# Performance work log

Hardware: AMD Instinct MI355X
Metric: run time of the kernel (lower is better)

The kernel has to match this reference:

```python
import jax, jax.numpy as jnp
import numpy as np

N_EMBD = 384
N_HEAD = 6
HEAD_SIZE = N_EMBD // N_HEAD  # 64
BLOCK = 64
EPS = 1e-5


def _layernorm(x, g, b):
    mu = jnp.mean(x, axis=-1, keepdims=True)
    var = jnp.mean(jnp.square(x - mu), axis=-1, keepdims=True)
    return (x - mu) * jax.lax.rsqrt(var + EPS) * g + b


def setup_inputs() -> dict:
    key = jax.random.key(0)
    ks = jax.random.split(key, 12)
    s = 0.02
    return {
        "x": jax.random.normal(ks[0], (1024, BLOCK, N_EMBD), dtype=jnp.float32),
        "ln1_g": jnp.ones((N_EMBD,), jnp.float32),
        "ln1_b": jnp.zeros((N_EMBD,), jnp.float32),
        "Wq": jax.random.normal(ks[1], (N_HEAD, N_EMBD, HEAD_SIZE), jnp.float32) * s,
        "Wk": jax.random.normal(ks[2], (N_HEAD, N_EMBD, HEAD_SIZE), jnp.float32) * s,
        "Wv": jax.random.normal(ks[3], (N_HEAD, N_EMBD, HEAD_SIZE), jnp.float32) * s,
        "Wo": jax.random.normal(ks[4], (N_EMBD, N_EMBD), jnp.float32) * s,
        "bo": jnp.zeros((N_EMBD,), jnp.float32),
        "ln2_g": jnp.ones((N_EMBD,), jnp.float32),
        "ln2_b": jnp.zeros((N_EMBD,), jnp.float32),
        "W1": jax.random.normal(ks[5], (N_EMBD, 4 * N_EMBD), jnp.float32) * s,
        "b1": jnp.zeros((4 * N_EMBD,), jnp.float32),
        "W2": jax.random.normal(ks[6], (4 * N_EMBD, N_EMBD), jnp.float32) * s,
        "b2": jnp.zeros((N_EMBD,), jnp.float32),
    }


def reference(x, ln1_g, ln1_b, Wq, Wk, Wv, Wo, bo, ln2_g, ln2_b, W1, b1, W2, b2):
    B, T, C = x.shape
    # --- multi-head causal self-attention on ln1(x) ---
    xn = _layernorm(x, ln1_g, ln1_b)
    q = jnp.einsum('btc,hcd->bhtd', xn, Wq)
    k = jnp.einsum('btc,hcd->bhtd', xn, Wk)
    v = jnp.einsum('btc,hcd->bhtd', xn, Wv)
    scale = HEAD_SIZE ** -0.5
    att = jnp.einsum('bhtd,bhsd->bhts', q, k) * scale
    causal = jnp.tril(jnp.ones((T, T), bool))
    att = jnp.where(causal, att, -jnp.inf)
    att = jax.nn.softmax(att, axis=-1)  # dropout is identity at eval
    out = jnp.einsum('bhts,bhsd->bhtd', att, v)
    out = out.transpose(0, 2, 1, 3).reshape(B, T, C)  # concat heads
    x = x + out @ Wo + bo
    # --- feed-forward on ln2(x) ---
    xn2 = _layernorm(x, ln2_g, ln2_b)
    h = jax.nn.relu(xn2 @ W1 + b1)
    x = x + h @ W2 + b2
    return x
```

## Files before the change

### kernel.cpp

```cpp
#include <hip/hip_runtime.h>

#define TT 64
#define CC 384
#define NH 6
#define HID 1536
#define LDX 392
#define LDH 72
#define LDM 200

typedef __bf16 bf16x8 __attribute__((ext_vector_type(8)));
typedef float f32x4 __attribute__((ext_vector_type(4)));
typedef unsigned short us8 __attribute__((ext_vector_type(8)));

#define MFMA(a, b, c) __builtin_amdgcn_mfma_f32_16x16x32_bf16(a, b, c, 0, 0, 0)

static __device__ __forceinline__ unsigned short f2bf(float f) {
  unsigned u = __builtin_bit_cast(unsigned, f);
  u += 0x7FFFu + ((u >> 16) & 1u);
  return (unsigned short)(u >> 16);
}
static __device__ __forceinline__ float bf2f(unsigned short h) {
  unsigned u = ((unsigned)h) << 16;
  return __builtin_bit_cast(float, u);
}
static __device__ __forceinline__ bf16x8 ld8(const unsigned short* p) {
  return __builtin_bit_cast(bf16x8, *reinterpret_cast<const us8*>(p));
}

__global__ void prep_w(const float* __restrict__ Wq, const float* __restrict__ Wk,
                       const float* __restrict__ Wv, const float* __restrict__ Wo,
                       const float* __restrict__ W1, const float* __restrict__ W2,
                       unsigned short* __restrict__ ws) {
  const int T0 = 1152 * 384;
  const int T1 = T0 + 384 * 384;
  const int T2 = T1 + 1536 * 384;
  const int T3 = T2 + 384 * 1536;
  for (int i = blockIdx.x * blockDim.x + threadIdx.x; i < T3; i += gridDim.x * blockDim.x) {
    float v;
    if (i < T0) {
      int n = i / 384, k = i % 384;
      int hh = n / 192, j = n % 192;
      const float* W = (j < 64) ? Wq : (j < 128) ? Wk : Wv;
      int d = (j < 64) ? j : (j < 128) ? j - 64 : j - 128;
      v = W[((size_t)hh * 384 + k) * 64 + d];
    } else if (i < T1) {
      int i2 = i - T0; int n = i2 / 384, k = i2 % 384;
      v = Wo[(size_t)k * 384 + n];
    } else if (i < T2) {
      int i2 = i - T1; int n = i2 / 384, k = i2 % 384;
      v = W1[(size_t)k * 1536 + n];
    } else {
      int i2 = i - T2; int n = i2 / 1536, k = i2 % 1536;
      v = W2[(size_t)k * 384 + n];
    }
    ws[i] = f2bf(v);
  }
}

__global__ __launch_bounds__(256, 2)
void attn_fwd(const float* __restrict__ x,
              const float* __restrict__ ln1g, const float* __restrict__ ln1b,
              const float* __restrict__ bo,
              const unsigned short* __restrict__ Wqkv,
              const unsigned short* __restrict__ WoT,
              float* __restrict__ x2) {
  __shared__ unsigned short sXN[TT * LDX];
  __shared__ unsigned short sHEAD[3 * TT * LDH];
  unsigned short* sQ = sHEAD;
  unsigned short* sK = sHEAD + TT * LDH;
  unsigned short* sV = sHEAD + 2 * TT * LDH;

  const int b = blockIdx.x;
  const int tid = threadIdx.x;
  const int wv = tid >> 6;
  const int ln = tid & 63;
  const int l16 = ln & 15;
  const int lg = ln >> 4;
  const float* xb = x + (size_t)b * TT * CC;
  const f32x4 Z4 = {0.f, 0.f, 0.f, 0.f};

#pragma unroll 1
  for (int r = wv * 16; r < wv * 16 + 16; ++r) {
    float v[6], s = 0.f, sq = 0.f;
#pragma unroll
    for (int j = 0; j < 6; ++j) { v[j] = xb[r * CC + ln + 64 * j]; s += v[j]; sq += v[j] * v[j]; }
#pragma unroll
    for (int off = 32; off; off >>= 1) { s += __shfl_xor(s, off); sq += __shfl_xor(sq, off); }
    float mu = s * (1.f / CC);
    float rs = rsqrtf(sq * (1.f / CC) - mu * mu + 1e-5f);
#pragma unroll
    for (int j = 0; j < 6; ++j) {
      int c = ln + 64 * j;
      sXN[r * LDX + c] = f2bf((v[j] - mu) * rs * ln1g[c] + ln1b[c]);
    }
  }
  __syncthreads();

  f32x4 pacc[4][6];
#pragma unroll
  for (int m = 0; m < 4; ++m)
#pragma unroll
    for (int c = 0; c < 6; ++c) pacc[m][c] = Z4;

  const unsigned short* prow[6];
#pragma unroll
  for (int c = 0; c < 6; ++c)
    prow[c] = WoT + (size_t)(wv * 96 + c * 16 + l16) * CC + 8 * lg;

#pragma unroll 1
  for (int h = 0; h < NH; ++h) {
    const unsigned short* wrow[3];
#pragma unroll
    for (int c = 0; c < 3; ++c)
      wrow[c] = Wqkv + (size_t)(h * 192 + wv * 48 + c * 16 + l16) * CC + 8 * lg;

    f32x4 qacc[4][3];
#pragma unroll
    for (int m = 0; m < 4; ++m)
#pragma unroll
      for (int c = 0; c < 3; ++c) qacc[m][c] = Z4;

    bf16x8 bpre[2][3];
#pragma unroll
    for (int c = 0; c < 3; ++c) bpre[0][c] = ld8(wrow[c] + 0);
#pragma unroll
    for (int c = 0; c < 3; ++c) bpre[1][c] = ld8(wrow[c] + 32);
#pragma unroll
    for (int kk = 0; kk < CC; kk += 32) {
      const int slot = (kk >> 5) & 1;
      bf16x8 bcur[3];
#pragma unroll
      for (int c = 0; c < 3; ++c) bcur[c] = bpre[slot][c];
      if (kk + 64 < CC) {
#pragma unroll
        for (int c = 0; c < 3; ++c) bpre[slot][c] = ld8(wrow[c] + kk + 64);
      }
      bf16x8 a[4];
#pragma unroll
      for (int m = 0; m < 4; ++m)
        a[m] = ld8(&sXN[(m * 16 + l16) * LDX + kk + 8 * lg]);
      __builtin_amdgcn_s_setprio(1);
#pragma unroll
      for (int c = 0; c < 3; ++c)
#pragma unroll
        for (int m = 0; m < 4; ++m) qacc[m][c] = MFMA(a[m], bcur[c], qacc[m][c]);
      __builtin_amdgcn_s_setprio(0);
    }
    __syncthreads();
#pragma unroll
    for (int m = 0; m < 4; ++m)
#pragma unroll
      for (int c = 0; c < 3; ++c) {
        int n = wv * 48 + c * 16 + l16;
#pragma unroll
        for (int rg = 0; rg < 4; ++rg) {
          int t = m * 16 + lg * 4 + rg;
          unsigned short bv = f2bf(qacc[m][c][rg]);
          if (n < 64) sQ[t * LDH + n] = bv;
          else if (n < 128) sK[t * LDH + (n - 64)] = bv;
          else sV[(n - 128) * LDH + t] = bv;
        }
      }
    __syncthreads();

    f32x4 sacc[4];
#pragma unroll
    for (int c = 0; c < 4; ++c) sacc[c] = Z4;
#pragma unroll
    for (int kk = 0; kk < 64; kk += 32) {
      bf16x8 a = ld8(&sQ[(wv * 16 + l16) * LDH + kk + 8 * lg]);
#pragma unroll
      for (int c = 0; c < 4; ++c) {
        bf16x8 bb = ld8(&sK[(c * 16 + l16) * LDH + kk + 8 * lg]);
        sacc[c] = MFMA(a, bb, sacc[c]);
      }
    }
#pragma unroll
    for (int rg = 0; rg < 4; ++rg) {
      int row = wv * 16 + lg * 4 + rg;
      float e[4], mx = -1e30f;
#pragma unroll
      for (int c = 0; c < 4; ++c) {
        int col = c * 16 + l16;
        float vv = sacc[c][rg] * 0.125f;
        e[c] = (col <= row) ? vv : -1e30f;
        mx = fmaxf(mx, e[c]);
      }
#pragma unroll
      for (int off = 8; off; off >>= 1) mx = fmaxf(mx, __shfl_xor(mx, off));
      float sum = 0.f;
#pragma unroll
      for (int c = 0; c < 4; ++c) {
        int col = c * 16 + l16;
        e[c] = (col <= row) ? __expf(e[c] - mx) : 0.f;
        sum += e[c];
      }
#pragma unroll
      for (int off = 8; off; off >>= 1) sum += __shfl_xor(sum, off);
      float inv = 1.f / sum;
#pragma unroll
      for (int c = 0; c < 4; ++c)
        sQ[row * LDH + c * 16 + l16] = f2bf(e[c] * inv);
    }

    bf16x8 pb[2][6];
#pragma unroll
    for (int s2 = 0; s2 < 2; ++s2)
#pragma unroll
      for (int c = 0; c < 6; ++c)
        pb[s2][c] = ld8(prow[c] + h * 64 + 32 * s2);

    f32x4 oacc[4];
#pragma unroll
    for (int c = 0; c < 4; ++c) oacc[c] = Z4;
#pragma unroll
    for (int kk = 0; kk < 64; kk += 32) {
      bf16x8 a = ld8(&sQ[(wv * 16 + l16) * LDH + kk + 8 * lg]);
#pragma unroll
      for (int c = 0; c < 4; ++c) {
        bf16x8 bb = ld8(&sV[(c * 16 + l16) * LDH + kk + 8 * lg]);
        oacc[c] = MFMA(a, bb, oacc[c]);
      }
    }
    __syncthreads();
#pragma unroll
    for (int c = 0; c < 4; ++c)
#pragma unroll
      for (int rg = 0; rg < 4; ++rg) {
        int t = wv * 16 + lg * 4 + rg;
        sK[t * LDH + c * 16 + l16] = f2bf(oacc[c][rg]);
      }
    __syncthreads();

    __builtin_amdgcn_s_setprio(1);
#pragma unroll
    for (int kk = 0; kk < 64; kk += 32) {
      const int slot = kk >> 5;
      bf16x8 a[4];
#pragma unroll
      for (int m = 0; m < 4; ++m)
        a[m] = ld8(&sK[(m * 16 + l16) * LDH + kk + 8 * lg]);
#pragma unroll
      for (int c = 0; c < 6; ++c)
#pragma unroll
        for (int m = 0; m < 4; ++m) pacc[m][c] = MFMA(a[m], pb[slot][c], pacc[m][c]);
    }
    __builtin_amdgcn_s_setprio(0);
  }

  float* xo = x2 + (size_t)b * TT * CC;
#pragma unroll
  for (int m = 0; m < 4; ++m)
#pragma unroll
    for (int c = 0; c < 6; ++c) {
      int n = wv * 96 + c * 16 + l16;
      float bov = bo[n];
#pragma unroll
      for (int rg = 0; rg < 4; ++rg) {
        int t = m * 16 + lg * 4 + rg;
        xo[t * CC + n] = xb[t * CC + n] + pacc[m][c][rg] + bov;
      }
    }
}

__global__ __launch_bounds__(256, 2)
void mlp_fwd(const float* __restrict__ ln2g, const float* __restrict__ ln2b,
             const float* __restrict__ b1, const float* __restrict__ b2,
             const unsigned short* __restrict__ W1T,
             const unsigned short* __restrict__ W2T,
             float* xo) {
  __shared__ unsigned short sXN[TT * LDX];
  __shared__ unsigned short sH[TT * LDM];

  const int b = blockIdx.x;
  const int tid = threadIdx.x;
  const int wv = tid >> 6;
  const int ln = tid & 63;
  const int l16 = ln & 15;
  const int lg = ln >> 4;
  float* xb = xo + (size_t)b * TT * CC;
  const f32x4 Z4 = {0.f, 0.f, 0.f, 0.f};

#pragma unroll 1
  for (int r = wv * 16; r < wv * 16 + 16; ++r) {
    float v[6], s = 0.f, sq = 0.f;
#pragma unroll
    for (int j = 0; j < 6; ++j) { v[j] = xb[r * CC + ln + 64 * j]; s += v[j]; sq += v[j] * v[j]; }
#pragma unroll
    for (int off = 32; off; off >>= 1) { s += __shfl_xor(s, off); sq += __shfl_xor(sq, off); }
    float mu = s * (1.f / CC);
    float rs = rsqrtf(sq * (1.f / CC) - mu * mu + 1e-5f);
#pragma unroll
    for (int j = 0; j < 6; ++j) {
      int c = ln + 64 * j;
      sXN[r * LDX + c] = f2bf((v[j] - mu) * rs * ln2g[c] + ln2b[c]);
    }
  }
  __syncthreads();

  f32x4 macc[4][6];
#pragma unroll
  for (int m = 0; m < 4; ++m)
#pragma unroll
    for (int c = 0; c < 6; ++c) macc[m][c] = Z4;

  const unsigned short* w2row[6];
#pragma unroll
  for (int c = 0; c < 6; ++c)
    w2row[c] = W2T + (size_t)(wv * 96 + c * 16 + l16) * HID + 8 * lg;

#pragma unroll 1
  for (int ch = 0; ch < 8; ++ch) {
    const unsigned short* w1row[3];
#pragma unroll
    for (int c = 0; c < 3; ++c)
      w1row[c] = W1T + (size_t)(ch * 192 + wv * 48 + c * 16 + l16) * CC + 8 * lg;

    f32x4 hacc[4][3];
#pragma unroll
    for (int m = 0; m < 4; ++m)
#pragma unroll
      for (int c = 0; c < 3; ++c) hacc[m][c] = Z4;

    bf16x8 bpre[2][3];
#pragma unroll
    for (int c = 0; c < 3; ++c) bpre[0][c] = ld8(w1row[c] + 0);
#pragma unroll
    for (int c = 0; c < 3; ++c) bpre[1][c] = ld8(w1row[c] + 32);
#pragma unroll
    for (int kk = 0; kk < CC; kk += 32) {
      const int slot = (kk >> 5) & 1;
      bf16x8 bcur[3];
#pragma unroll
      for (int c = 0; c < 3; ++c) bcur[c] = bpre[slot][c];
      if (kk + 64 < CC) {
#pragma unroll
        for (int c = 0; c < 3; ++c) bpre[slot][c] = ld8(w1row[c] + kk + 64);
      }
      bf16x8 a[4];
#pragma unroll
      for (int m = 0; m < 4; ++m)
        a[m] = ld8(&sXN[(m * 16 + l16) * LDX + kk + 8 * lg]);
      __builtin_amdgcn_s_setprio(1);
#pragma unroll
      for (int c = 0; c < 3; ++c)
#pragma unroll
        for (int m = 0; m < 4; ++m) hacc[m][c] = MFMA(a[m], bcur[c], hacc[m][c]);
      __builtin_amdgcn_s_setprio(0);
    }
    __syncthreads();
#pragma unroll
    for (int m = 0; m < 4; ++m)
#pragma unroll
      for (int c = 0; c < 3; ++c) {
        int nl = wv * 48 + c * 16 + l16;
        float b1v = b1[ch * 192 + nl];
#pragma unroll
        for (int rg = 0; rg < 4; ++rg) {
          int t = m * 16 + lg * 4 + rg;
          sH[t * LDM + nl] = f2bf(fmaxf(hacc[m][c][rg] + b1v, 0.f));
        }
      }
    __syncthreads();

    bf16x8 b2p[6];
#pragma unroll
    for (int c = 0; c < 6; ++c) b2p[c] = ld8(w2row[c] + ch * 192);
#pragma unroll
    for (int kk = 0; kk < 192; kk += 32) {
      bf16x8 b2n[6];
      if (kk + 32 < 192) {
#pragma unroll
        for (int c = 0; c < 6; ++c) b2n[c] = ld8(w2row[c] + ch * 192 + kk + 32);
      }
      bf16x8 a[4];
#pragma unroll
      for (int m = 0; m < 4; ++m)
        a[m] = ld8(&sH[(m * 16 + l16) * LDM + kk + 8 * lg]);
      __builtin_amdgcn_s_setprio(1);
#pragma unroll
      for (int c = 0; c < 6; ++c)
#pragma unroll
        for (int m = 0; m < 4; ++m) macc[m][c] = MFMA(a[m], b2p[c], macc[m][c]);
      __builtin_amdgcn_s_setprio(0);
      if (kk + 32 < 192) {
#pragma unroll
        for (int c = 0; c < 6; ++c) b2p[c] = b2n[c];
      }
    }
  }
#pragma unroll
  for (int m = 0; m < 4; ++m)
#pragma unroll
    for (int c = 0; c < 6; ++c) {
      int n = wv * 96 + c * 16 + l16;
      float b2v = b2[n];
#pragma unroll
      for (int rg = 0; rg < 4; ++rg) {
        int t = m * 16 + lg * 4 + rg;
        size_t idx = (size_t)t * CC + n;
        float x2v = xb[idx];
        xb[idx] = x2v + macc[m][c][rg] + b2v;
      }
    }
}

extern "C" void kernel_launch(void* const* d_in, const int* in_sizes, int n_in,
                              void* d_out, int out_size, void* d_ws, size_t ws_size,
                              hipStream_t stream) {
  const float* x    = (const float*)d_in[0];
  const float* ln1g = (const float*)d_in[1];
  const float* ln1b = (const float*)d_in[2];
  const float* Wq   = (const float*)d_in[3];
  const float* Wk   = (const float*)d_in[4];
  const float* Wv   = (const float*)d_in[5];
  const float* Wo   = (const float*)d_in[6];
  const float* bo   = (const float*)d_in[7];
  const float* ln2g = (const float*)d_in[8];
  const float* ln2b = (const float*)d_in[9];
  const float* W1   = (const float*)d_in[10];
  const float* b1   = (const float*)d_in[11];
  const float* W2   = (const float*)d_in[12];
  const float* b2   = (const float*)d_in[13];
  unsigned short* ws = (unsigned short*)d_ws;

  const size_t need = (size_t)(1152 * 384 + 384 * 384 + 1536 * 384 + 384 * 1536) * 2;
  if (ws_size < need) return;

  hipLaunchKernelGGL(prep_w, dim3(1024), dim3(256), 0, stream, Wq, Wk, Wv, Wo, W1, W2, ws);

  const unsigned short* Wqkv = ws;
  const unsigned short* WoT  = ws + 1152 * 384;
  const unsigned short* W1T  = WoT + 384 * 384;
  const unsigned short* W2T  = W1T + 1536 * 384;
  int nblk = in_sizes[0] / (TT * CC);

  hipLaunchKernelGGL(attn_fwd, dim3(nblk), dim3(256), 0, stream,
                     x, ln1g, ln1b, bo, Wqkv, WoT, (float*)d_out);
  hipLaunchKernelGGL(mlp_fwd, dim3(nblk), dim3(256), 0, stream,
                     ln2g, ln2b, b1, b2, W1T, W2T, (float*)d_out);
}
```

Baseline: 512.2 us.

## Restructure MLP kernel to 8 waves with double-buffered LDS weight staging

The MLP kernel moves from 4 to 8 waves per block and switches hidden chunks from 8×192 to 6×256. Weight tiles now stream through per-wave double-buffered LDS slots using global_load_lds with XOR-swizzled layout and explicit vmcnt waits, replacing direct register prefetch from global memory. The aim is to overlap weight fetches with MFMA work and raise latency hiding through more waves. In exchange the block uses much more LDS (an extra 64KB), which may limit occupancy. The s_setprio hints in the attention kernel are also removed.

```diff
diff --git a/kernel.cpp b/kernel.cpp
--- a/kernel.cpp
+++ b/kernel.cpp
@@ -6,13 +6,14 @@
 #define HID 1536
 #define LDX 392
 #define LDH 72
-#define LDM 200
+#define LDS_H 264
 
 typedef __bf16 bf16x8 __attribute__((ext_vector_type(8)));
 typedef float f32x4 __attribute__((ext_vector_type(4)));
 typedef unsigned short us8 __attribute__((ext_vector_type(8)));
 
 #define MFMA(a, b, c) __builtin_amdgcn_mfma_f32_16x16x32_bf16(a, b, c, 0, 0, 0)
+#define WAITVM(N) asm volatile("s_waitcnt vmcnt(" #N ")" ::: "memory")
 
 static __device__ __forceinline__ unsigned short f2bf(float f) {
   unsigned u = __builtin_bit_cast(unsigned, f);
@@ -25,6 +26,11 @@
 }
 static __device__ __forceinline__ bf16x8 ld8(const unsigned short* p) {
   return __builtin_bit_cast(bf16x8, *reinterpret_cast<const us8*>(p));
+}
+static __device__ __forceinline__ void glds16(const unsigned short* g, unsigned short* l) {
+  __builtin_amdgcn_global_load_lds(
+      (const __attribute__((address_space(1))) void*)g,
+      (__attribute__((address_space(3))) void*)l, 16, 0, 0);
 }
 
 __global__ void prep_w(const float* __restrict__ Wq, const float* __restrict__ Wk,
@@ -139,12 +145,10 @@
 #pragma unroll
       for (int m = 0; m < 4; ++m)
         a[m] = ld8(&sXN[(m * 16 + l16) * LDX + kk + 8 * lg]);
-      __builtin_amdgcn_s_setprio(1);
 #pragma unroll
       for (int c = 0; c < 3; ++c)
 #pragma unroll
         for (int m = 0; m < 4; ++m) qacc[m][c] = MFMA(a[m], bcur[c], qacc[m][c]);
-      __builtin_amdgcn_s_setprio(0);
     }
     __syncthreads();
 #pragma unroll
@@ -232,7 +236,6 @@
       }
     __syncthreads();
 
-    __builtin_amdgcn_s_setprio(1);
 #pragma unroll
     for (int kk = 0; kk < 64; kk += 32) {
       const int slot = kk >> 5;
@@ -245,7 +248,6 @@
 #pragma unroll
         for (int m = 0; m < 4; ++m) pacc[m][c] = MFMA(a[m], pb[slot][c], pacc[m][c]);
     }
-    __builtin_amdgcn_s_setprio(0);
   }
 
   float* xo = x2 + (size_t)b * TT * CC;
@@ -263,14 +265,15 @@
     }
 }
 
-__global__ __launch_bounds__(256, 2)
+__global__ __launch_bounds__(512, 2)
 void mlp_fwd(const float* __restrict__ ln2g, const float* __restrict__ ln2b,
              const float* __restrict__ b1, const float* __restrict__ b2,
              const unsigned short* __restrict__ W1T,
              const unsigned short* __restrict__ W2T,
              float* xo) {
   __shared__ unsigned short sXN[TT * LDX];
-  __shared__ unsigned short sH[TT * LDM];
+  __shared__ unsigned short sH[TT * LDS_H];
+  __shared__ unsigned short sW[8 * 4096];
 
   const int b = blockIdx.x;
   const int tid = threadIdx.x;
@@ -280,9 +283,10 @@
   const int lg = ln >> 4;
   float* xb = xo + (size_t)b * TT * CC;
   const f32x4 Z4 = {0.f, 0.f, 0.f, 0.f};
-
-#pragma unroll 1
-  for (int r = wv * 16; r < wv * 16 + 16; ++r) {
+  unsigned short* myW = sW + (wv << 12);
+
+#pragma unroll 1
+  for (int r = wv * 8; r < wv * 8 + 8; ++r) {
     float v[6], s = 0.f, sq = 0.f;
 #pragma unroll
     for (int j = 0; j < 6; ++j) { v[j] = xb[r * CC + ln + 64 * j]; s += v[j]; sq += v[j] * v[j]; }
@@ -298,102 +302,113 @@
   }
   __syncthreads();
 
-  f32x4 macc[4][6];
+  const int w1_row = (wv << 5) + (ln >> 3);
+  const int w1_kp0 = (((ln & 7) ^ (ln >> 3)) << 3);
+  const int w2_row = wv * 48 + (ln >> 2);
+  const int w2_kp0 = ((((ln & 3) ^ ((ln >> 3) & 3))) << 3);
+
+  f32x4 macc[4][3];
 #pragma unroll
   for (int m = 0; m < 4; ++m)
 #pragma unroll
-    for (int c = 0; c < 6; ++c) macc[m][c] = Z4;
-
-  const unsigned short* w2row[6];
-#pragma unroll
-  for (int c = 0; c < 6; ++c)
-    w2row[c] = W2T + (size_t)(wv * 96 + c * 16 + l16) * HID + 8 * lg;
-
-#pragma unroll 1
-  for (int ch = 0; ch < 8; ++ch) {
-    const unsigned short* w1row[3];
-#pragma unroll
-    for (int c = 0; c < 3; ++c)
-      w1row[c] = W1T + (size_t)(ch * 192 + wv * 48 + c * 16 + l16) * CC + 8 * lg;
-
-    f32x4 hacc[4][3];
+    for (int c = 0; c < 3; ++c) macc[m][c] = Z4;
+
+#pragma unroll 1
+  for (int ch = 0; ch < 6; ++ch) {
+    f32x4 hacc[4][2];
 #pragma unroll
     for (int m = 0; m < 4; ++m)
 #pragma unroll
-      for (int c = 0; c < 3; ++c) hacc[m][c] = Z4;
-
-    bf16x8 bpre[2][3];
-#pragma unroll
-    for (int c = 0; c < 3; ++c) bpre[0][c] = ld8(w1row[c] + 0);
-#pragma unroll
-    for (int c = 0; c < 3; ++c) bpre[1][c] = ld8(w1row[c] + 32);
-#pragma unroll
-    for (int kk = 0; kk < CC; kk += 32) {
-      const int slot = (kk >> 5) & 1;
-      bf16x8 bcur[3];
-#pragma unroll
-      for (int c = 0; c < 3; ++c) bcur[c] = bpre[slot][c];
-      if (kk + 64 < CC) {
-#pragma unroll
-        for (int c = 0; c < 3; ++c) bpre[slot][c] = ld8(w1row[c] + kk + 64);
-      }
-      bf16x8 a[4];
-#pragma unroll
-      for (int m = 0; m < 4; ++m)
-        a[m] = ld8(&sXN[(m * 16 + l16) * LDX + kk + 8 * lg]);
-      __builtin_amdgcn_s_setprio(1);
-#pragma unroll
-      for (int c = 0; c < 3; ++c)
-#pragma unroll
-        for (int m = 0; m < 4; ++m) hacc[m][c] = MFMA(a[m], bcur[c], hacc[m][c]);
-      __builtin_amdgcn_s_setprio(0);
-    }
-    __syncthreads();
+      for (int c = 0; c < 2; ++c) hacc[m][c] = Z4;
+
+    {
+      const unsigned short* g = W1T + (size_t)(ch * 256 + w1_row) * CC + 0 * 64 + w1_kp0;
+      unsigned short* d = myW + 0 * 2048;
+#pragma unroll
+      for (int j = 0; j < 4; ++j) glds16(g + (size_t)(j * 8) * CC, d + (j << 9));
+    }
+    int cb = 0;
+#pragma unroll 1
+    for (int s = 0; s < 6; ++s) {
+      if (s < 5) {
+        const unsigned short* g = W1T + (size_t)(ch * 256 + w1_row) * CC + (s + 1) * 64 + w1_kp0;
+        unsigned short* d = myW + (cb ^ 1) * 2048;
+#pragma unroll
+        for (int j = 0; j < 4; ++j) glds16(g + (size_t)(j * 8) * CC, d + (j << 9));
+        WAITVM(4);
+      } else {
+        WAITVM(0);
+      }
+#pragma unroll
+      for (int kk2 = 0; kk2 < 2; ++kk2) {
+        bf16x8 a[4];
+#pragma unroll
+        for (int m = 0; m < 4; ++m)
+          a[m] = ld8(&sXN[(m * 16 + l16) * LDX + s * 64 + kk2 * 32 + 8 * lg]);
+#pragma unroll
+        for (int c = 0; c < 2; ++c) {
+          int rloc = (c << 4) + l16;
+          bf16x8 bb = ld8(&myW[cb * 2048 + rloc * 64 + ((kk2 * 32 + 8 * lg) ^ ((l16 & 7) << 3))]);
+#pragma unroll
+          for (int m = 0; m < 4; ++m) hacc[m][c] = MFMA(a[m], bb, hacc[m][c]);
+        }
+      }
+      cb ^= 1;
+    }
+    __syncthreads();
+
+    {
+      const unsigned short* g = W2T + (size_t)w2_row * HID + ch * 256 + 0 * 32 + w2_kp0;
+      unsigned short* d = myW + 0 * 1536;
+#pragma unroll
+      for (int j = 0; j < 3; ++j) glds16(g + (size_t)(j * 16) * HID, d + (j << 9));
+    }
 #pragma unroll
     for (int m = 0; m < 4; ++m)
 #pragma unroll
-      for (int c = 0; c < 3; ++c) {
-        int nl = wv * 48 + c * 16 + l16;
-        float b1v = b1[ch * 192 + nl];
+      for (int c = 0; c < 2; ++c) {
+        int nl = (wv << 5) + (c << 4) + l16;
+        float b1v = b1[ch * 256 + nl];
 #pragma unroll
         for (int rg = 0; rg < 4; ++rg) {
           int t = m * 16 + lg * 4 + rg;
-          sH[t * LDM + nl] = f2bf(fmaxf(hacc[m][c][rg] + b1v, 0.f));
+          sH[t * LDS_H + nl] = f2bf(fmaxf(hacc[m][c][rg] + b1v, 0.f));
         }
       }
     __syncthreads();
 
-    bf16x8 b2p[6];
-#pragma unroll
-    for (int c = 0; c < 6; ++c) b2p[c] = ld8(w2row[c] + ch * 192);
-#pragma unroll
-    for (int kk = 0; kk < 192; kk += 32) {
-      bf16x8 b2n[6];
-      if (kk + 32 < 192) {
-#pragma unroll
-        for (int c = 0; c < 6; ++c) b2n[c] = ld8(w2row[c] + ch * 192 + kk + 32);
+    cb = 0;
+#pragma unroll 1
+    for (int s = 0; s < 8; ++s) {
+      if (s < 7) {
+        const unsigned short* g = W2T + (size_t)w2_row * HID + ch * 256 + (s + 1) * 32 + w2_kp0;
+        unsigned short* d = myW + (cb ^ 1) * 1536;
+#pragma unroll
+        for (int j = 0; j < 3; ++j) glds16(g + (size_t)(j * 16) * HID, d + (j << 9));
+        WAITVM(3);
+      } else {
+        WAITVM(0);
       }
       bf16x8 a[4];
 #pragma unroll
       for (int m = 0; m < 4; ++m)
-        a[m] = ld8(&sH[(m * 16 + l16) * LDM + kk + 8 * lg]);
-      __builtin_amdgcn_s_setprio(1);
-#pragma unroll
-      for (int c = 0; c < 6; ++c)
-#pragma unroll
-        for (int m = 0; m < 4; ++m) macc[m][c] = MFMA(a[m], b2p[c], macc[m][c]);
-      __builtin_amdgcn_s_setprio(0);
-      if (kk + 32 < 192) {
-#pragma unroll
-        for (int c = 0; c < 6; ++c) b2p[c] = b2n[c];
-      }
+        a[m] = ld8(&sH[(m * 16 + l16) * LDS_H + s * 32 + 8 * lg]);
+#pragma unroll
+      for (int c = 0; c < 3; ++c) {
+        int rloc = (c << 4) + l16;
+        bf16x8 bb = ld8(&myW[cb * 1536 + rloc * 32 + ((8 * lg) ^ (((rloc >> 1) & 3) << 3))]);
+#pragma unroll
+        for (int m = 0; m < 4; ++m) macc[m][c] = MFMA(a[m], bb, macc[m][c]);
+      }
+      cb ^= 1;
     }
   }
+
 #pragma unroll
   for (int m = 0; m < 4; ++m)
 #pragma unroll
-    for (int c = 0; c < 6; ++c) {
-      int n = wv * 96 + c * 16 + l16;
+    for (int c = 0; c < 3; ++c) {
+      int n = wv * 48 + c * 16 + l16;
       float b2v = b2[n];
 #pragma unroll
       for (int rg = 0; rg < 4; ++rg) {
@@ -437,6 +452,6 @@
 
   hipLaunchKernelGGL(attn_fwd, dim3(nblk), dim3(256), 0, stream,
                      x, ln1g, ln1b, bo, Wqkv, WoT, (float*)d_out);
-  hipLaunchKernelGGL(mlp_fwd, dim3(nblk), dim3(256), 0, stream,
+  hipLaunchKernelGGL(mlp_fwd, dim3(nblk), dim3(512), 0, stream,
                      ln2g, ln2b, b1, b2, W1T, W2T, (float*)d_out);
 }
```

Result: faster. 468.4 us (-8.6%).

## Restructure MLP kernel to 8 waves with swizzled LDS layout and smaller hidden chunks

Applied to the files above, without the earlier changes.

The MLP kernel moves from 4 to 8 waves per block (512 threads). Each wave now owns 16 hidden columns per 128-wide hidden chunk (12 chunks) and 48 output columns, which halves the per-wave accumulators and is meant to raise occupancy and latency hiding. The padded row-major LDS tiles become an XOR-swizzled fragment layout so the MFMA operand loads avoid bank conflicts. The trade-offs are more chunk iterations, more barriers per block, and each wave reloading the same A fragments from LDS.

```diff
diff --git a/kernel.cpp b/kernel.cpp
--- a/kernel.cpp
+++ b/kernel.cpp
@@ -6,7 +6,6 @@
 #define HID 1536
 #define LDX 392
 #define LDH 72
-#define LDM 200
 
 typedef __bf16 bf16x8 __attribute__((ext_vector_type(8)));
 typedef float f32x4 __attribute__((ext_vector_type(4)));
@@ -263,14 +262,14 @@
     }
 }
 
-__global__ __launch_bounds__(256, 2)
+__global__ __launch_bounds__(512, 4)
 void mlp_fwd(const float* __restrict__ ln2g, const float* __restrict__ ln2b,
              const float* __restrict__ b1, const float* __restrict__ b2,
              const unsigned short* __restrict__ W1T,
              const unsigned short* __restrict__ W2T,
              float* xo) {
-  __shared__ unsigned short sXN[TT * LDX];
-  __shared__ unsigned short sH[TT * LDM];
+  __shared__ unsigned short sXN[24576];
+  __shared__ unsigned short sH[8192];
 
   const int b = blockIdx.x;
   const int tid = threadIdx.x;
@@ -280,9 +279,10 @@
   const int lg = ln >> 4;
   float* xb = xo + (size_t)b * TT * CC;
   const f32x4 Z4 = {0.f, 0.f, 0.f, 0.f};
+  const int rx = (l16 ^ lg) << 3;
 
 #pragma unroll 1
-  for (int r = wv * 16; r < wv * 16 + 16; ++r) {
+  for (int r = wv * 8; r < wv * 8 + 8; ++r) {
     float v[6], s = 0.f, sq = 0.f;
 #pragma unroll
     for (int j = 0; j < 6; ++j) { v[j] = xb[r * CC + ln + 64 * j]; s += v[j]; sq += v[j] * v[j]; }
@@ -290,110 +290,99 @@
     for (int off = 32; off; off >>= 1) { s += __shfl_xor(s, off); sq += __shfl_xor(sq, off); }
     float mu = s * (1.f / CC);
     float rs = rsqrtf(sq * (1.f / CC) - mu * mu + 1e-5f);
+    int m = r >> 4, row16 = r & 15;
 #pragma unroll
     for (int j = 0; j < 6; ++j) {
       int c = ln + 64 * j;
-      sXN[r * LDX + c] = f2bf((v[j] - mu) * rs * ln2g[c] + ln2b[c]);
+      int sl = c >> 5, ks = (c >> 3) & 3, off = c & 7;
+      sXN[(((m * 12 + sl) * 4 + ks) * 16 + (row16 ^ ks)) * 8 + off] =
+          f2bf((v[j] - mu) * rs * ln2g[c] + ln2b[c]);
     }
   }
   __syncthreads();
 
-  f32x4 macc[4][6];
+  f32x4 macc[4][3];
 #pragma unroll
   for (int m = 0; m < 4; ++m)
 #pragma unroll
-    for (int c = 0; c < 6; ++c) macc[m][c] = Z4;
-
-  const unsigned short* w2row[6];
-#pragma unroll
-  for (int c = 0; c < 6; ++c)
-    w2row[c] = W2T + (size_t)(wv * 96 + c * 16 + l16) * HID + 8 * lg;
+    for (int c = 0; c < 3; ++c) macc[m][c] = Z4;
 
 #pragma unroll 1
-  for (int ch = 0; ch < 8; ++ch) {
-    const unsigned short* w1row[3];
-#pragma unroll
-    for (int c = 0; c < 3; ++c)
-      w1row[c] = W1T + (size_t)(ch * 192 + wv * 48 + c * 16 + l16) * CC + 8 * lg;
-
-    f32x4 hacc[4][3];
-#pragma unroll
-    for (int m = 0; m < 4; ++m)
-#pragma unroll
-      for (int c = 0; c < 3; ++c) hacc[m][c] = Z4;
-
-    bf16x8 bpre[2][3];
-#pragma unroll
-    for (int c = 0; c < 3; ++c) bpre[0][c] = ld8(w1row[c] + 0);
-#pragma unroll
-    for (int c = 0; c < 3; ++c) bpre[1][c] = ld8(w1row[c] + 32);
-#pragma unroll
-    for (int kk = 0; kk < CC; kk += 32) {
-      const int slot = (kk >> 5) & 1;
-      bf16x8 bcur[3];
-#pragma unroll
-      for (int c = 0; c < 3; ++c) bcur[c] = bpre[slot][c];
-      if (kk + 64 < CC) {
-#pragma unroll
-        for (int c = 0; c < 3; ++c) bpre[slot][c] = ld8(w1row[c] + kk + 64);
-      }
+  for (int ch = 0; ch < 12; ++ch) {
+    f32x4 hacc[4];
+#pragma unroll
+    for (int m = 0; m < 4; ++m) hacc[m] = Z4;
+
+    const unsigned short* w1p = W1T + (size_t)(ch * 128 + wv * 16 + l16) * CC + 8 * lg;
+    bf16x8 bpre[2];
+    bpre[0] = ld8(w1p);
+    bpre[1] = ld8(w1p + 32);
+#pragma unroll
+    for (int sl = 0; sl < 12; ++sl) {
+      const int slot = sl & 1;
+      bf16x8 bcur = bpre[slot];
+      if (sl + 2 < 12) bpre[slot] = ld8(w1p + (sl + 2) * 32);
       bf16x8 a[4];
 #pragma unroll
       for (int m = 0; m < 4; ++m)
-        a[m] = ld8(&sXN[(m * 16 + l16) * LDX + kk + 8 * lg]);
+        a[m] = ld8(&sXN[((m * 48 + sl * 4 + lg) << 7) + rx]);
       __builtin_amdgcn_s_setprio(1);
 #pragma unroll
+      for (int m = 0; m < 4; ++m) hacc[m] = MFMA(a[m], bcur, hacc[m]);
+      __builtin_amdgcn_s_setprio(0);
+    }
+
+    float b1v = b1[ch * 128 + wv * 16 + l16];
+    const unsigned short* w2p = W2T + (size_t)(wv * 48 + l16) * HID + ch * 128 + 8 * lg;
+    bf16x8 c2[3];
+#pragma unroll
+    for (int c = 0; c < 3; ++c) c2[c] = ld8(w2p + (size_t)(c * 16) * HID);
+
+    __syncthreads();
+
+    {
+      int nl = wv * 16 + l16;
+      int slh = nl >> 5, ks = (nl >> 3) & 3, off = nl & 7;
+#pragma unroll
+      for (int m = 0; m < 4; ++m)
+#pragma unroll
+        for (int rg = 0; rg < 4; ++rg) {
+          int row16 = lg * 4 + rg;
+          sH[(((m * 4 + slh) * 4 + ks) * 16 + (row16 ^ ks)) * 8 + off] =
+              f2bf(fmaxf(hacc[m][rg] + b1v, 0.f));
+        }
+    }
+    __syncthreads();
+
+#pragma unroll
+    for (int sl = 0; sl < 4; ++sl) {
+      bf16x8 a2[4];
+#pragma unroll
+      for (int m = 0; m < 4; ++m)
+        a2[m] = ld8(&sH[((m * 16 + sl * 4 + lg) << 7) + rx]);
+      bf16x8 nxt[3];
+      if (sl < 3) {
+#pragma unroll
+        for (int c = 0; c < 3; ++c) nxt[c] = ld8(w2p + (size_t)(c * 16) * HID + (sl + 1) * 32);
+      }
+      __builtin_amdgcn_s_setprio(1);
+#pragma unroll
       for (int c = 0; c < 3; ++c)
 #pragma unroll
-        for (int m = 0; m < 4; ++m) hacc[m][c] = MFMA(a[m], bcur[c], hacc[m][c]);
+        for (int m = 0; m < 4; ++m) macc[m][c] = MFMA(a2[m], c2[c], macc[m][c]);
       __builtin_amdgcn_s_setprio(0);
-    }
-    __syncthreads();
-#pragma unroll
-    for (int m = 0; m < 4; ++m)
-#pragma unroll
-      for (int c = 0; c < 3; ++c) {
-        int nl = wv * 48 + c * 16 + l16;
-        float b1v = b1[ch * 192 + nl];
-#pragma unroll
-        for (int rg = 0; rg < 4; ++rg) {
-          int t = m * 16 + lg * 4 + rg;
-          sH[t * LDM + nl] = f2bf(fmaxf(hacc[m][c][rg] + b1v, 0.f));
-        }
-      }
-    __syncthreads();
-
-    bf16x8 b2p[6];
-#pragma unroll
-    for (int c = 0; c < 6; ++c) b2p[c] = ld8(w2row[c] + ch * 192);
-#pragma unroll
-    for (int kk = 0; kk < 192; kk += 32) {
-      bf16x8 b2n[6];
-      if (kk + 32 < 192) {
-#pragma unroll
-        for (int c = 0; c < 6; ++c) b2n[c] = ld8(w2row[c] + ch * 192 + kk + 32);
-      }
-      bf16x8 a[4];
-#pragma unroll
-      for (int m = 0; m < 4; ++m)
-        a[m] = ld8(&sH[(m * 16 + l16) * LDM + kk + 8 * lg]);
-      __builtin_amdgcn_s_setprio(1);
-#pragma unroll
-      for (int c = 0; c < 6; ++c)
-#pragma unroll
-        for (int m = 0; m < 4; ++m) macc[m][c] = MFMA(a[m], b2p[c], macc[m][c]);
-      __builtin_amdgcn_s_setprio(0);
-      if (kk + 32 < 192) {
-#pragma unroll
-        for (int c = 0; c < 6; ++c) b2p[c] = b2n[c];
+      if (sl < 3) {
+#pragma unroll
+        for (int c = 0; c < 3; ++c) c2[c] = nxt[c];
       }
     }
   }
+
 #pragma unroll
   for (int m = 0; m < 4; ++m)
 #pragma unroll
-    for (int c = 0; c < 6; ++c) {
-      int n = wv * 96 + c * 16 + l16;
+    for (int c = 0; c < 3; ++c) {
+      int n = wv * 48 + c * 16 + l16;
       float b2v = b2[n];
 #pragma unroll
       for (int rg = 0; rg < 4; ++rg) {
@@ -437,6 +426,6 @@
 
   hipLaunchKernelGGL(attn_fwd, dim3(nblk), dim3(256), 0, stream,
                      x, ln1g, ln1b, bo, Wqkv, WoT, (float*)d_out);
-  hipLaunchKernelGGL(mlp_fwd, dim3(nblk), dim3(256), 0, stream,
+  hipLaunchKernelGGL(mlp_fwd, dim3(nblk), dim3(512), 0, stream,
                      ln2g, ln2b, b1, b2, W1T, W2T, (float*)d_out);
 }
```

Result: faster. 484.9 us (-5.3%).
